# Performance work log

Hardware: AMD Instinct MI355X
Metric: run time of the kernel (lower is better)

Reference implementation:

```python
import jax, jax.numpy as jnp
import numpy as np

B, C, H, W = 8, 512, 64, 64
D = C // 8  # qk_downscale = 8


def setup_inputs() -> dict:
    key = jax.random.key(0)
    k1, k2, k3, k4, k5 = jax.random.split(key, 5)
    scale = 1.0 / np.sqrt(C)
    return {
        "x": jax.random.normal(k1, (B, C, H, W), dtype=jnp.float32),
        "Wq": jax.random.normal(k2, (D, C), dtype=jnp.float32) * scale,
        "Wk": jax.random.normal(k3, (D, C), dtype=jnp.float32) * scale,
        "Wv": jax.random.normal(k4, (C, C), dtype=jnp.float32) * scale,
        "gamma": jax.random.normal(k5, (1,), dtype=jnp.float32) * 0.1,
    }


def reference(x, Wq, Wk, Wv, gamma):
    b, c, h, w = x.shape
    n = h * w
    xf = x.reshape(b, c, n)                      # [B, C, N]
    # 1x1 Conv1d (bias=False) == channel matmul
    q = jnp.einsum('dc,bcn->bdn', Wq, xf)        # [B, D, N]
    k = jnp.einsum('dc,bcn->bdn', Wk, xf)        # [B, D, N]
    v = jnp.einsum('oc,bcn->bon', Wv, xf)        # [B, C, N]
    # torch.bmm(q.transpose(1,2), k) -> [B, N, N], unscaled
    qk = jnp.einsum('bdn,bdm->bnm', q, k)        # [B, N, N]
    # nn.Softmax(dim=1): normalize over the FIRST N axis (rows)
    attn = jax.nn.softmax(qk, axis=1)            # [B, N, N]
    # torch.bmm(v, qk_softmaxed) -> [B, C, N]
    out = gamma * jnp.einsum('bcn,bnm->bcm', v, attn) + xf
    return out.reshape(b, c, h, w)
```

## Files before the change

kernel.cpp:

```cpp
#include <hip/hip_runtime.h>
#include <math.h>
#include <stdint.h>

constexpr int Bn = 8;
constexpr int Cn = 512;
constexpr int Dn = 64;
constexpr int Nn = 4096;

typedef __bf16 bf16x8 __attribute__((ext_vector_type(8)));
typedef float  f32x16 __attribute__((ext_vector_type(16)));

typedef const __attribute__((address_space(1))) uint8_t* gptr_t;
typedef __attribute__((address_space(3))) uint8_t*       lptr_t;

static __device__ __forceinline__ uint32_t pkbf(float a, float b) {
    union { float f; uint32_t u; } x, y; x.f = a; y.f = b;
    uint32_t ra = (x.u + 0x7fffu + ((x.u >> 16) & 1u)) >> 16;
    uint32_t rb = (y.u + 0x7fffu + ((y.u >> 16) & 1u)) & 0xffff0000u;
    return ra | rb;
}

static __device__ __forceinline__ uint32_t cvt2(float a, float b) {
    union { __bf16 h[2]; uint32_t u; } p;
    p.h[0] = (__bf16)a; p.h[1] = (__bf16)b;
    return p.u;
}

static __device__ __forceinline__ float fexp2(float x) {
#if __has_builtin(__builtin_amdgcn_exp2f)
    return __builtin_amdgcn_exp2f(x);
#else
    return exp2f(x);
#endif
}

__global__ __launch_bounds__(256) void convert_w(
    const float* __restrict__ Wq, const float* __restrict__ Wk,
    const float* __restrict__ Wv, uint16_t* __restrict__ wb)
{
    int g = blockIdx.x * 256 + threadIdx.x;
    int tile = g >> 9;
    int s    = g & 511;
    int Ob = tile >> 3, cT = tile & 7;
    int ch = s >> 6,  o  = s & 63;
    const float* src;
    if (Ob == 0)       src = Wq + (size_t)o * Cn;
    else if (Ob == 1)  src = Wk + (size_t)o * Cn;
    else               src = Wv + (size_t)((Ob - 2) * 64 + o) * Cn;
    src += cT * 64 + ch * 8;
    float4 a = ((const float4*)src)[0];
    float4 c = ((const float4*)src)[1];
    uint4 u;
    u.x = pkbf(a.x, a.y); u.y = pkbf(a.z, a.w);
    u.z = pkbf(c.x, c.y); u.w = pkbf(c.z, c.w);
    *(uint4*)(wb + (size_t)g * 8) = u;
}

__global__ __launch_bounds__(256) void convert_x(
    const float* __restrict__ X, uint16_t* __restrict__ xt)
{
    __shared__ float Xs[64][68];
    const int ntile = blockIdx.x;
    const int cT    = blockIdx.y;
    const int b     = blockIdx.z;
    const int t  = threadIdx.x;
    const int lr = t >> 2;
    const int lc = (t & 3) << 4;
    const float* src = X + ((size_t)b * Cn + cT * 64 + lr) * Nn + ntile * 64 + lc;
    float4 v0 = ((const float4*)src)[0];
    float4 v1 = ((const float4*)src)[1];
    float4 v2 = ((const float4*)src)[2];
    float4 v3 = ((const float4*)src)[3];
    *(float4*)&Xs[lr][lc +  0] = v0;
    *(float4*)&Xs[lr][lc +  4] = v1;
    *(float4*)&Xs[lr][lc +  8] = v2;
    *(float4*)&Xs[lr][lc + 12] = v3;
    __syncthreads();
    const int nT = ntile >> 2, nb = ntile & 3;
    const size_t base = (((size_t)b * 16 + nT) * 8 + cT) * 8;
    #pragma unroll
    for (int ss = 0; ss < 2; ++ss) {
        int s  = t + ss * 256;
        int ch = s >> 6, nl = s & 63;
        uint4 u;
        u.x = pkbf(Xs[ch * 8 + 0][nl], Xs[ch * 8 + 1][nl]);
        u.y = pkbf(Xs[ch * 8 + 2][nl], Xs[ch * 8 + 3][nl]);
        u.z = pkbf(Xs[ch * 8 + 4][nl], Xs[ch * 8 + 5][nl]);
        u.w = pkbf(Xs[ch * 8 + 6][nl], Xs[ch * 8 + 7][nl]);
        *(uint4*)(xt + ((base + ch) * 256 + nb * 64 + nl) * 8) = u;
    }
}

__global__ __launch_bounds__(256, 2) void gemm_qkv(
    const uint16_t* __restrict__ wb, const uint16_t* __restrict__ xt,
    uint16_t* __restrict__ qt, uint16_t* __restrict__ kt,
    uint16_t* __restrict__ vt)
{
    __shared__ __align__(16) uint8_t Wlds[2][8192];
    __shared__ __align__(16) uint8_t Xlds[2][32768];
    const int nT = blockIdx.x;
    const int oB = blockIdx.y;
    const int b  = blockIdx.z;
    const int t    = threadIdx.x;
    const int lane = t & 63;
    const int wq   = __builtin_amdgcn_readfirstlane(t >> 6);
    const int mrow = lane & 31;
    const int qh   = lane >> 5;
    const uint8_t* wtiles = (const uint8_t*)wb + (size_t)oB * 8 * 8192;
    const uint8_t* xtiles = (const uint8_t*)xt + (((size_t)b * 16 + nT) * 8) * 32768;
    const bool isv = (oB >= 2);

    f32x16 acc[2][2];
    #pragma unroll
    for (int i = 0; i < 2; ++i)
        #pragma unroll
        for (int j = 0; j < 2; ++j)
            #pragma unroll
            for (int r = 0; r < 16; ++r) acc[i][j][r] = 0.f;

    auto STAGE = [&](int bf, int cT) {
        #pragma unroll
        for (int i2 = 0; i2 < 2; ++i2) {
            int s = wq * 2 + i2;
            __builtin_amdgcn_global_load_lds(
                (gptr_t)(wtiles + cT * 8192 + s * 1024 + lane * 16),
                (lptr_t)(Wlds[bf] + s * 1024), 16, 0, 0);
        }
        #pragma unroll
        for (int i8 = 0; i8 < 8; ++i8) {
            int s = wq * 8 + i8;
            __builtin_amdgcn_global_load_lds(
                (gptr_t)(xtiles + cT * 32768 + s * 1024 + lane * 16),
                (lptr_t)(Xlds[bf] + s * 1024), 16, 0, 0);
        }
    };

    STAGE(0, 0);
    __syncthreads();

    for (int cT = 0; cT < 8; ++cT) {
        const int cur = cT & 1;
        if (cT < 7) STAGE(cur ^ 1, cT + 1);
        const uint8_t* Wb = Wlds[cur];
        const uint8_t* Xb = Xlds[cur];
        #pragma unroll
        for (int i = 0; i < 4; ++i) {
            int ch = 2 * i + qh;
            bf16x8 wf0 = *(const bf16x8*)(Wb + ch * 1024 + mrow * 16);
            bf16x8 wf1 = *(const bf16x8*)(Wb + ch * 1024 + (32 + mrow) * 16);
            bf16x8 xf0 = *(const bf16x8*)(Xb + ch * 4096 + (wq * 64 + mrow) * 16);
            bf16x8 xf1 = *(const bf16x8*)(Xb + ch * 4096 + (wq * 64 + 32 + mrow) * 16);
            if (!isv) {
                acc[0][0] = __builtin_amdgcn_mfma_f32_32x32x16_bf16(wf0, xf0, acc[0][0], 0, 0, 0);
                acc[0][1] = __builtin_amdgcn_mfma_f32_32x32x16_bf16(wf0, xf1, acc[0][1], 0, 0, 0);
                acc[1][0] = __builtin_amdgcn_mfma_f32_32x32x16_bf16(wf1, xf0, acc[1][0], 0, 0, 0);
                acc[1][1] = __builtin_amdgcn_mfma_f32_32x32x16_bf16(wf1, xf1, acc[1][1], 0, 0, 0);
            } else {
                acc[0][0] = __builtin_amdgcn_mfma_f32_32x32x16_bf16(xf0, wf0, acc[0][0], 0, 0, 0);
                acc[0][1] = __builtin_amdgcn_mfma_f32_32x32x16_bf16(xf0, wf1, acc[0][1], 0, 0, 0);
                acc[1][0] = __builtin_amdgcn_mfma_f32_32x32x16_bf16(xf1, wf0, acc[1][0], 0, 0, 0);
                acc[1][1] = __builtin_amdgcn_mfma_f32_32x32x16_bf16(xf1, wf1, acc[1][1], 0, 0, 0);
            }
        }
        __syncthreads();
    }

    if (!isv) {
        uint16_t* dst = (oB == 0) ? qt : kt;
        const float qs = (oB == 0) ? 1.4426950408889634f : 1.0f;
        #pragma unroll
        for (int ot = 0; ot < 2; ++ot)
            #pragma unroll
            for (int ns = 0; ns < 2; ++ns) {
                int T = nT * 8 + wq * 2 + ns;
                size_t tb = ((size_t)b * 128 + T) * 2048;
                #pragma unroll
                for (int rr = 0; rr < 4; ++rr) {
                    uint2 u;
                    u.x = pkbf(qs * acc[ot][ns][4 * rr + 0], qs * acc[ot][ns][4 * rr + 1]);
                    u.y = pkbf(qs * acc[ot][ns][4 * rr + 2], qs * acc[ot][ns][4 * rr + 3]);
                    *(uint2*)(dst + tb + (size_t)(ot * 4 + rr) * 256 + mrow * 8 + 4 * qh) = u;
                }
            }
    } else {
        #pragma unroll
        for (int ns = 0; ns < 2; ++ns)
            #pragma unroll
            for (int ot = 0; ot < 2; ++ot) {
                int T = nT * 8 + wq * 2 + ns;
                int c_out = (oB - 2) * 64 + ot * 32 + mrow;
                size_t tb = ((size_t)b * 128 + T) * 16384;
                uint4 U0, U1;
                U0.x = pkbf(acc[ns][ot][ 0], acc[ns][ot][ 1]);
                U0.y = pkbf(acc[ns][ot][ 2], acc[ns][ot][ 3]);
                U0.z = pkbf(acc[ns][ot][ 4], acc[ns][ot][ 5]);
                U0.w = pkbf(acc[ns][ot][ 6], acc[ns][ot][ 7]);
                U1.x = pkbf(acc[ns][ot][ 8], acc[ns][ot][ 9]);
                U1.y = pkbf(acc[ns][ot][10], acc[ns][ot][11]);
                U1.z = pkbf(acc[ns][ot][12], acc[ns][ot][13]);
                U1.w = pkbf(acc[ns][ot][14], acc[ns][ot][15]);
                *(uint4*)(vt + tb + (size_t)qh      * 4096 + c_out * 8) = U0;
                *(uint4*)(vt + tb + (size_t)(2+qh)  * 4096 + c_out * 8) = U1;
            }
    }
}

__global__ __launch_bounds__(256, 2) void flash_attn(
    const uint16_t* __restrict__ qt, const uint16_t* __restrict__ kt,
    const uint16_t* __restrict__ vt, const float* __restrict__ X,
    const float* __restrict__ gamma, float* __restrict__ out)
{
    __shared__ __align__(16) uint8_t Vlds[2][32768];

    const int bid = blockIdx.x;
    const int b   = bid & 7;
    const int mB  = bid >> 3;

    const int t    = threadIdx.x;
    const int lane = t & 63;
    const int wq   = __builtin_amdgcn_readfirstlane(t >> 6);
    const int wm   = wq >> 1;
    const int wc   = wq & 1;
    const int mrow = lane & 31;
    const int qh   = lane >> 5;

    const uint8_t* kbase = (const uint8_t*)kt
        + ((size_t)b * 128 + (size_t)mB * 2 + wm) * 4096;
    const uint8_t* vbase = (const uint8_t*)vt + (size_t)b * 128 * 32768;
    const uint8_t* qbase = (const uint8_t*)qt + (size_t)b * 128 * 4096;

    bf16x8 kfr[4];
    #pragma unroll
    for (int i = 0; i < 4; ++i)
        kfr[i] = *(const bf16x8*)(kbase + (2 * i + qh) * 512 + mrow * 16);

    auto STAGE = [&](int bf, int T) {
        const uint8_t* vsrc = vbase + (size_t)T * 32768;
        #pragma unroll
        for (int i = 0; i < 8; ++i) {
            int s = wq * 8 + i;
            __builtin_amdgcn_global_load_lds((gptr_t)(vsrc + s * 1024 + lane * 16),
                                             (lptr_t)(Vlds[bf] + s * 1024), 16, 0, 0);
        }
    };

    bf16x8 qcur[4];
    #pragma unroll
    for (int i = 0; i < 4; ++i)
        qcur[i] = *(const bf16x8*)(qbase + (2 * i + qh) * 512 + mrow * 16);

    f32x16 acc[8];
    #pragma unroll
    for (int cf = 0; cf < 8; ++cf)
        #pragma unroll
        for (int r = 0; r < 16; ++r) acc[cf][r] = 0.f;
    float lrun = 0.f;

    constexpr float SBIAS = -86.5617024533378f;

    STAGE(0, 0);
    __syncthreads();

    for (int T = 0; T < 128; ++T) {
        if (T < 127) STAGE((T + 1) & 1, T + 1);
        bf16x8 qnext[4];
        if (T < 127) {
            const uint8_t* qsrc = qbase + (size_t)(T + 1) * 4096;
            #pragma unroll
            for (int i = 0; i < 4; ++i)
                qnext[i] = *(const bf16x8*)(qsrc + (2 * i + qh) * 512 + mrow * 16);
        }

        f32x16 S;
        #pragma unroll
        for (int r = 0; r < 16; ++r) S[r] = SBIAS;
        #pragma unroll
        for (int i = 0; i < 4; ++i)
            S = __builtin_amdgcn_mfma_f32_32x32x16_bf16(qcur[i], kfr[i], S, 0, 0, 0);

        union pu { uint32_t u[4]; bf16x8 v; };
        pu Pf0, Pf1;
        {
            float p[16];
            #pragma unroll
            for (int r = 0; r < 16; ++r) p[r] = fexp2(S[r]);
            float s0 = 0.f, s1 = 0.f, s2 = 0.f, s3 = 0.f;
            #pragma unroll
            for (int r = 0; r < 4; ++r) {
                s0 += p[r]; s1 += p[4 + r]; s2 += p[8 + r]; s3 += p[12 + r];
            }
            lrun += (s0 + s1) + (s2 + s3);
            #pragma unroll
            for (int j = 0; j < 4; ++j) Pf0.u[j] = cvt2(p[2 * j],     p[2 * j + 1]);
            #pragma unroll
            for (int j = 0; j < 4; ++j) Pf1.u[j] = cvt2(p[8 + 2 * j], p[8 + 2 * j + 1]);
        }

        const uint8_t* vb_ = Vlds[T & 1];
        #pragma unroll
        for (int cf = 0; cf < 8; ++cf) {
            int cloc = wc * 256 + cf * 32 + mrow;
            bf16x8 vfA = *(const bf16x8*)(vb_ + (size_t)qh       * 8192 + cloc * 16);
            bf16x8 vfC = *(const bf16x8*)(vb_ + (size_t)(2 + qh) * 8192 + cloc * 16);
            acc[cf] = __builtin_amdgcn_mfma_f32_32x32x16_bf16(vfA, Pf0.v, acc[cf], 0, 0, 0);
            acc[cf] = __builtin_amdgcn_mfma_f32_32x32x16_bf16(vfC, Pf1.v, acc[cf], 0, 0, 0);
        }

        #pragma unroll
        for (int i = 0; i < 4; ++i) qcur[i] = qnext[i];

        __syncthreads();
    }

    const float Lm  = lrun + __shfl_xor(lrun, 32);
    const float g   = gamma[0];
    const float scale = g / Lm;
    const float* xb = X   + (size_t)b * Cn * Nn;
    float*       ob = out + (size_t)b * Cn * Nn;
    const int m = mB * 64 + wm * 32 + mrow;
    #pragma unroll
    for (int cf = 0; cf < 8; ++cf)
        #pragma unroll
        for (int r = 0; r < 16; ++r) {
            int c = wc * 256 + cf * 32 + (r & 3) + 8 * (r >> 2) + 4 * qh;
            size_t idx = (size_t)c * Nn + m;
            ob[idx] = scale * acc[cf][r] + xb[idx];
        }
}

extern "C" void kernel_launch(void* const* d_in, const int* in_sizes, int n_in,
                              void* d_out, int out_size, void* d_ws, size_t ws_size,
                              hipStream_t stream)
{
    const float* x     = (const float*)d_in[0];
    const float* Wq    = (const float*)d_in[1];
    const float* Wk    = (const float*)d_in[2];
    const float* Wv    = (const float*)d_in[3];
    const float* gamma = (const float*)d_in[4];
    float* out = (float*)d_out;

    uint16_t* qt = (uint16_t*)d_ws;
    uint16_t* kt = qt + (size_t)2097152;
    uint16_t* vt = kt + (size_t)2097152;
    uint16_t* xt = vt + (size_t)16777216;
    uint16_t* wbuf = xt + (size_t)16777216;

    convert_w <<<dim3(160),       256, 0, stream>>>(Wq, Wk, Wv, wbuf);
    convert_x <<<dim3(64, 8, 8),  256, 0, stream>>>(x, xt);
    gemm_qkv  <<<dim3(16, 10, 8), 256, 0, stream>>>(wbuf, xt, qt, kt, vt);
    flash_attn<<<dim3(512),       256, 0, stream>>>(qt, kt, vt, x, gamma, out);
}
```

Baseline: 338.3 us.

## Halve LDS staging, load half of V directly to registers, interleave softmax with MFMAs

The QKV GEMM now stages half-size channel chunks (16 steps instead of 8) so LDS use drops and launch bounds allow 3 blocks per SM. In flash attention, only half of each V tile goes through LDS. The other half is loaded straight from global memory into registers. The exp/convert work for the second P fragment is split so it overlaps with the first batch of PV MFMAs, and s_setprio raises priority around the MFMA blocks. This aims to raise occupancy and hide softmax latency behind matrix work, at the cost of more VGPRs and uncoalesced-ish direct global V loads exposed to latency.

```diff
diff --git a/kernel.cpp b/kernel.cpp
--- a/kernel.cpp
+++ b/kernel.cpp
@@ -91,13 +91,13 @@
     }
 }
 
-__global__ __launch_bounds__(256, 2) void gemm_qkv(
+__global__ __launch_bounds__(256, 3) void gemm_qkv(
     const uint16_t* __restrict__ wb, const uint16_t* __restrict__ xt,
     uint16_t* __restrict__ qt, uint16_t* __restrict__ kt,
     uint16_t* __restrict__ vt)
 {
-    __shared__ __align__(16) uint8_t Wlds[2][8192];
-    __shared__ __align__(16) uint8_t Xlds[2][32768];
+    __shared__ __align__(16) uint8_t Wlds[2][4096];
+    __shared__ __align__(16) uint8_t Xlds[2][16384];
     const int nT = blockIdx.x;
     const int oB = blockIdx.y;
     const int b  = blockIdx.z;
@@ -118,34 +118,29 @@
             #pragma unroll
             for (int r = 0; r < 16; ++r) acc[i][j][r] = 0.f;
 
-    auto STAGE = [&](int bf, int cT) {
-        #pragma unroll
-        for (int i2 = 0; i2 < 2; ++i2) {
-            int s = wq * 2 + i2;
+    auto STAGE = [&](int bf, int s) {
+        const int cT = s >> 1, h = s & 1;
+        __builtin_amdgcn_global_load_lds(
+            (gptr_t)(wtiles + cT * 8192 + h * 4096 + t * 16),
+            (lptr_t)(Wlds[bf] + t * 16), 16, 0, 0);
+        #pragma unroll
+        for (int i = 0; i < 4; ++i)
             __builtin_amdgcn_global_load_lds(
-                (gptr_t)(wtiles + cT * 8192 + s * 1024 + lane * 16),
-                (lptr_t)(Wlds[bf] + s * 1024), 16, 0, 0);
-        }
-        #pragma unroll
-        for (int i8 = 0; i8 < 8; ++i8) {
-            int s = wq * 8 + i8;
-            __builtin_amdgcn_global_load_lds(
-                (gptr_t)(xtiles + cT * 32768 + s * 1024 + lane * 16),
-                (lptr_t)(Xlds[bf] + s * 1024), 16, 0, 0);
-        }
+                (gptr_t)(xtiles + cT * 32768 + h * 16384 + (i * 256 + t) * 16),
+                (lptr_t)(Xlds[bf] + (i * 256 + t) * 16), 16, 0, 0);
     };
 
     STAGE(0, 0);
     __syncthreads();
 
-    for (int cT = 0; cT < 8; ++cT) {
-        const int cur = cT & 1;
-        if (cT < 7) STAGE(cur ^ 1, cT + 1);
+    for (int s = 0; s < 16; ++s) {
+        const int cur = s & 1;
+        if (s < 15) STAGE(cur ^ 1, s + 1);
         const uint8_t* Wb = Wlds[cur];
         const uint8_t* Xb = Xlds[cur];
         #pragma unroll
-        for (int i = 0; i < 4; ++i) {
-            int ch = 2 * i + qh;
+        for (int i2 = 0; i2 < 2; ++i2) {
+            int ch = 2 * i2 + qh;
             bf16x8 wf0 = *(const bf16x8*)(Wb + ch * 1024 + mrow * 16);
             bf16x8 wf1 = *(const bf16x8*)(Wb + ch * 1024 + (32 + mrow) * 16);
             bf16x8 xf0 = *(const bf16x8*)(Xb + ch * 4096 + (wq * 64 + mrow) * 16);
@@ -210,7 +205,7 @@
     const uint16_t* __restrict__ vt, const float* __restrict__ X,
     const float* __restrict__ gamma, float* __restrict__ out)
 {
-    __shared__ __align__(16) uint8_t Vlds[2][32768];
+    __shared__ __align__(16) uint8_t Vlds[2][16384];
 
     const int bid = blockIdx.x;
     const int b   = bid & 7;
@@ -237,8 +232,8 @@
     auto STAGE = [&](int bf, int T) {
         const uint8_t* vsrc = vbase + (size_t)T * 32768;
         #pragma unroll
-        for (int i = 0; i < 8; ++i) {
-            int s = wq * 8 + i;
+        for (int i = 0; i < 4; ++i) {
+            int s = wq * 4 + i;
             __builtin_amdgcn_global_load_lds((gptr_t)(vsrc + s * 1024 + lane * 16),
                                              (lptr_t)(Vlds[bf] + s * 1024), 16, 0, 0);
         }
@@ -263,6 +258,14 @@
 
     for (int T = 0; T < 128; ++T) {
         if (T < 127) STAGE((T + 1) & 1, T + 1);
+
+        const uint8_t* vbg = vbase + (size_t)T * 32768 + (size_t)(2 + qh) * 8192
+                             + (size_t)wc * 4096;
+        bf16x8 vfC[8];
+        #pragma unroll
+        for (int cf = 0; cf < 8; ++cf)
+            vfC[cf] = *(const bf16x8*)(vbg + (cf * 32 + mrow) * 16);
+
         bf16x8 qnext[4];
         if (T < 127) {
             const uint8_t* qsrc = qbase + (size_t)(T + 1) * 4096;
@@ -274,37 +277,54 @@
         f32x16 S;
         #pragma unroll
         for (int r = 0; r < 16; ++r) S[r] = SBIAS;
+        __builtin_amdgcn_s_setprio(1);
         #pragma unroll
         for (int i = 0; i < 4; ++i)
             S = __builtin_amdgcn_mfma_f32_32x32x16_bf16(qcur[i], kfr[i], S, 0, 0, 0);
+        __builtin_amdgcn_s_setprio(0);
 
         union pu { uint32_t u[4]; bf16x8 v; };
-        pu Pf0, Pf1;
+
+        pu Pf0;
+        float p0[8];
+        #pragma unroll
+        for (int r = 0; r < 8; ++r) p0[r] = fexp2(S[r]);
         {
-            float p[16];
-            #pragma unroll
-            for (int r = 0; r < 16; ++r) p[r] = fexp2(S[r]);
-            float s0 = 0.f, s1 = 0.f, s2 = 0.f, s3 = 0.f;
-            #pragma unroll
-            for (int r = 0; r < 4; ++r) {
-                s0 += p[r]; s1 += p[4 + r]; s2 += p[8 + r]; s3 += p[12 + r];
-            }
-            lrun += (s0 + s1) + (s2 + s3);
-            #pragma unroll
-            for (int j = 0; j < 4; ++j) Pf0.u[j] = cvt2(p[2 * j],     p[2 * j + 1]);
-            #pragma unroll
-            for (int j = 0; j < 4; ++j) Pf1.u[j] = cvt2(p[8 + 2 * j], p[8 + 2 * j + 1]);
-        }
-
-        const uint8_t* vb_ = Vlds[T & 1];
+            float s0 = 0.f, s1 = 0.f;
+            #pragma unroll
+            for (int r = 0; r < 4; ++r) { s0 += p0[r]; s1 += p0[4 + r]; }
+            lrun += s0 + s1;
+        }
+        #pragma unroll
+        for (int j = 0; j < 4; ++j) Pf0.u[j] = cvt2(p0[2 * j], p0[2 * j + 1]);
+
+        const uint8_t* vb_ = Vlds[T & 1] + (size_t)qh * 8192 + (size_t)wc * 4096;
+        __builtin_amdgcn_s_setprio(1);
         #pragma unroll
         for (int cf = 0; cf < 8; ++cf) {
-            int cloc = wc * 256 + cf * 32 + mrow;
-            bf16x8 vfA = *(const bf16x8*)(vb_ + (size_t)qh       * 8192 + cloc * 16);
-            bf16x8 vfC = *(const bf16x8*)(vb_ + (size_t)(2 + qh) * 8192 + cloc * 16);
+            bf16x8 vfA = *(const bf16x8*)(vb_ + (cf * 32 + mrow) * 16);
             acc[cf] = __builtin_amdgcn_mfma_f32_32x32x16_bf16(vfA, Pf0.v, acc[cf], 0, 0, 0);
-            acc[cf] = __builtin_amdgcn_mfma_f32_32x32x16_bf16(vfC, Pf1.v, acc[cf], 0, 0, 0);
-        }
+        }
+        __builtin_amdgcn_s_setprio(0);
+
+        pu Pf1;
+        float p1[8];
+        #pragma unroll
+        for (int r = 0; r < 8; ++r) p1[r] = fexp2(S[8 + r]);
+        {
+            float s0 = 0.f, s1 = 0.f;
+            #pragma unroll
+            for (int r = 0; r < 4; ++r) { s0 += p1[r]; s1 += p1[4 + r]; }
+            lrun += s0 + s1;
+        }
+        #pragma unroll
+        for (int j = 0; j < 4; ++j) Pf1.u[j] = cvt2(p1[2 * j], p1[2 * j + 1]);
+
+        __builtin_amdgcn_s_setprio(1);
+        #pragma unroll
+        for (int cf = 0; cf < 8; ++cf)
+            acc[cf] = __builtin_amdgcn_mfma_f32_32x32x16_bf16(vfC[cf], Pf1.v, acc[cf], 0, 0, 0);
+        __builtin_amdgcn_s_setprio(0);
 
         #pragma unroll
         for (int i = 0; i < 4; ++i) qcur[i] = qnext[i];
```

After: 354.0 us. 1.05x slower.
